# Optimization experiments

Hardware: AMD Instinct MI355X
Metric: run time of the kernel (lower is better)

The kernel has to match this reference:

```python
import jax, jax.numpy as jnp
import numpy as np

B, S, C = 128, 512, 128


def setup_inputs() -> dict:
    key = jax.random.key(0)
    k1, k2, k3, k4, k5 = jax.random.split(key, 5)
    emissions = jax.random.normal(k1, (B, S, C), dtype=jnp.float32)
    tags = jax.random.randint(k2, (B, S), 0, C, dtype=jnp.int64)
    mask = jnp.ones((B, S), dtype=bool)  # mask[:,0] must be True
    transitions = jax.random.normal(k3, (C, C), dtype=jnp.float32)
    start_transitions = jax.random.normal(k4, (C,), dtype=jnp.float32)
    end_transitions = jax.random.normal(k5, (C,), dtype=jnp.float32)
    return {"emissions": emissions, "tags": tags, "mask": mask,
            "transitions": transitions, "start_transitions": start_transitions,
            "end_transitions": end_transitions}


def _gold_score(emissions, tags, mask, transitions, start_t, end_t):
    # score of the gold tag path, fully vectorized over time
    b = jnp.arange(emissions.shape[0])
    score = start_t[tags[:, 0]] + emissions[b, 0, tags[:, 0]]            # [B]
    emit_t = jnp.take_along_axis(emissions, tags[..., None], axis=2)[..., 0]  # [B,S]
    trans_t = transitions[tags[:, :-1], tags[:, 1:]]                     # [B,S-1]
    score = score + jnp.sum((emit_t[:, 1:] + trans_t) * mask[:, 1:].astype(emissions.dtype), axis=1)
    last_idx = jnp.sum(mask.astype(jnp.int32), axis=1) - 1               # [B]
    last_tags = jnp.take_along_axis(tags, last_idx[:, None], axis=1)[:, 0]
    return score + end_t[last_tags]


def _partition(emissions, mask, transitions, start_t, end_t):
    # forward algorithm: sequential logsumexp recurrence via lax.scan
    alpha0 = start_t[None, :] + emissions[:, 0]                          # [B,C]

    def step(alpha, inp):
        emit_t, mask_t = inp                                             # [B,C], [B]
        score = alpha[:, :, None] + transitions[None] + emit_t[:, None, :]  # [B,C,C]
        new_alpha = jax.nn.logsumexp(score, axis=1)                      # [B,C]
        alpha = jnp.where(mask_t[:, None], new_alpha, alpha)
        return alpha, None

    xs = (jnp.moveaxis(emissions[:, 1:], 1, 0), mask[:, 1:].T)           # [S-1,B,C], [S-1,B]
    alpha, _ = jax.lax.scan(step, alpha0, xs)
    return jax.nn.logsumexp(alpha + end_t[None, :], axis=1)              # [B]


def reference(emissions, tags, mask, transitions, start_transitions, end_transitions):
    gold = _gold_score(emissions, tags, mask, transitions, start_transitions, end_transitions)
    part = _partition(emissions, mask, transitions, start_transitions, end_transitions)
    return -(gold - part).mean()
```

## Files before the change

kernel.cpp:

```cpp
#include <hip/hip_runtime.h>

#define BB 128
#define SS 512
#define CC 128

__device__ __forceinline__ void barrier_lgkm() {
    asm volatile("s_waitcnt lgkmcnt(0)" ::: "memory");
    __builtin_amdgcn_s_barrier();
}

__device__ __forceinline__ float lanebcast(float v, int i) {
    return __int_as_float(__builtin_amdgcn_readlane(__float_as_int(v), i));
}

__global__ __launch_bounds__(512, 1)
void crf_half_kernel(const float* __restrict__ emissions,
                     const int*   __restrict__ tags,
                     const float* __restrict__ transitions,
                     const float* __restrict__ start_t,
                     const float* __restrict__ end_t,
                     float* __restrict__ ws)
{
    const int  blk = blockIdx.x;
    const bool isF = (blk < BB);
    const int  b   = isF ? blk : (blk - BB);
    const int  tid = threadIdx.x;
    const int  wv  = tid >> 6;
    const int  q   = wv & 3;
    const int  h   = wv >> 2;
    const int  l   = tid & 63;
    const int  u0  = l & 31;
    const int  j   = h * 64 + l;
    const int  i   = q * 32 + u0;

    float*  gold = ws;
    float*  xf   = ws + BB;
    float*  xb   = xf + BB * CC;
    double* Mf   = (double*)(xb + BB * CC);
    double* Mb   = Mf + BB;

    __shared__ float slot[2][4][CC];
    __shared__ float redg[8];

    const float* em_b = emissions + (size_t)b * SS * CC;

    float Ereg[32];
    {
        const float* Tb = transitions + (isF ? ((size_t)(q * 32) * CC + j)
                                             : ((size_t)j * CC + q * 32));
        const int us = isF ? CC : 1;
        #pragma unroll
        for (int t2 = 0; t2 < 32; ++t2) Ereg[t2] = __expf(Tb[(size_t)t2 * us]);
        #pragma unroll
        for (int t2 = 0; t2 < 32; ++t2) asm volatile("" : "+v"(Ereg[t2]));
    }

    float p = isF ? __expf(start_t[i] + em_b[i])
                  : __expf(end_t[i] + em_b[(size_t)(SS - 1) * CC + i]);
    double M = 0.0;

    const ptrdiff_t em_stride = isF ? (ptrdiff_t)CC : -(ptrdiff_t)CC;
    const float* em_base = em_b + i + (isF ? 3 * CC : 508 * CC);
    float ld0 = em_base[-2 * em_stride];
    float ld1 = em_base[-1 * em_stride];
    float ld2 = em_base[0];

#define SUBSTEP(T_, PAR, IS_BRIDGE) do {                                      \
        float a0=0.f, a1=0.f, a2=0.f, a3=0.f;                                 \
        _Pragma("unroll")                                                     \
        for (int uu = 0; uu < 8; ++uu) {                                      \
            a0 = fmaf(lanebcast(p, 4*uu+0), Ereg[4*uu+0], a0);                \
            a1 = fmaf(lanebcast(p, 4*uu+1), Ereg[4*uu+1], a1);                \
            a2 = fmaf(lanebcast(p, 4*uu+2), Ereg[4*uu+2], a2);                \
            a3 = fmaf(lanebcast(p, 4*uu+3), Ereg[4*uu+3], a3);                \
        }                                                                     \
        slot[PAR][q][j] = (a0 + a1) + (a2 + a3);            \
        float ev = __expf(ld0);                      \
        ld0 = ld1; ld1 = ld2;                                                 \
        ld2 = em_base[(ptrdiff_t)(T_) * em_stride];                           \
        barrier_lgkm();                                                       \
        float s = (slot[PAR][0][i] + slot[PAR][1][i]) +                       \
                  (slot[PAR][2][i] + slot[PAR][3][i]);        \
        float pn = s * ev;                                                    \
        if (!(IS_BRIDGE) && ((T_) & 3) == 1) {                                \
            float r = (slot[PAR][0][0] + slot[PAR][1][0]) +                   \
                      (slot[PAR][2][0] + slot[PAR][3][0]);                    \
            float lr = __logf(r);           \
            M += (double)lr;                                                  \
            pn *= __expf(-lr);                                                \
        }                                                                     \
        if (IS_BRIDGE) pn = s;              \
        p = pn;                                                               \
    } while (0)

    #pragma unroll 1
    for (int t = 1; t < 255; t += 2) {
        SUBSTEP(t,     1, false);
        SUBSTEP(t + 1, 0, false);
    }
    SUBSTEP(255, 1, false);
    if (isF) SUBSTEP(256, 0, true);
#undef SUBSTEP

    if (h == 0 && l < 32) (isF ? xf : xb)[(size_t)b * CC + i] = p;
    if (tid == 0) { if (isF) Mf[b] = M; else Mb[b] = M; }

    if (!isF) {
        const int* tg = tags + b * SS;
        const int t  = tid;
        const int ct = tg[t];
        float g;
        if (t == 0) g = start_t[ct] + em_b[ct] + end_t[tg[SS - 1]];
        else        g = em_b[(size_t)t * CC + ct] + transitions[tg[t - 1] * CC + ct];
        #pragma unroll
        for (int off = 32; off; off >>= 1) g += __shfl_down(g, off);
        if (l == 0) redg[wv] = g;
        __syncthreads();
        if (tid == 0) {
            float gg = 0.f;
            #pragma unroll
            for (int k2 = 0; k2 < 8; ++k2) gg += redg[k2];
            gold[b] = gg;
        }
    }
}

__global__ __launch_bounds__(1024)
void crf_final_kernel(const float* __restrict__ ws, float* __restrict__ out)
{
    const float*  gold = ws;
    const float*  xf   = ws + BB;
    const float*  xb   = xf + BB * CC;
    const double* Mf   = (const double*)(xb + BB * CC);
    const double* Mb   = Mf + BB;

    const int tid = threadIdx.x;
    const int b   = tid >> 3;
    const int g   = tid & 7;

    const float* xa = xf + (size_t)b * CC + g * 16;
    const float* xc = xb + (size_t)b * CC + g * 16;
    float z = 0.f;
    #pragma unroll
    for (int k = 0; k < 16; ++k) z = fmaf(xa[k], xc[k], z);
    z += __shfl_down(z, 4);
    z += __shfl_down(z, 2);
    z += __shfl_down(z, 1);

    __shared__ float d_s[BB];
    __shared__ float red[2];
    if (g == 0) {
        double part = Mf[b] + Mb[b] + (double)__logf(z);
        d_s[b] = gold[b] - (float)part;
    }
    __syncthreads();

    float v = (tid < BB) ? d_s[tid] : 0.f;
    #pragma unroll
    for (int off = 32; off; off >>= 1) v += __shfl_down(v, off);
    if (tid == 0 || tid == 64) red[tid >> 6] = v;
    __syncthreads();
    if (tid == 0) out[0] = -(red[0] + red[1]) / (float)BB;
}

extern "C" void kernel_launch(void* const* d_in, const int* in_sizes, int n_in,
                              void* d_out, int out_size, void* d_ws, size_t ws_size,
                              hipStream_t stream) {
    const float* emissions   = (const float*)d_in[0];
    const int*   tags        = (const int*)d_in[1];
    const float* transitions = (const float*)d_in[3];
    const float* start_t     = (const float*)d_in[4];
    const float* end_t       = (const float*)d_in[5];
    float* out = (float*)d_out;
    float* ws  = (float*)d_ws;

    crf_half_kernel<<<2 * BB, 512, 0, stream>>>(emissions, tags, transitions,
                                                start_t, end_t, ws);
    crf_final_kernel<<<1, 1024, 0, stream>>>(ws, out);
}
```

Measured before the change: 178.8 us.

## Halve workgroup to 256 threads with 64-wide K split per wave

Each block now runs 4 waves instead of 8. Each wave holds 64 exp-transition values and reduces over 64 source states instead of 32, so the cross-wave LDS reduction after the barrier sums 2 partials instead of 4. The emission exp multiply moves before the LDS store, and the gold-score loop processes two timesteps per thread. The aim is a cheaper barrier and reduction per step, at the cost of a longer serial FMA/readlane chain per step and more registers.

Result: faster. 175.1 us (-2.0%).

```diff
diff --git a/kernel.cpp b/kernel.cpp
--- a/kernel.cpp
+++ b/kernel.cpp
@@ -13,7 +13,7 @@
     return __int_as_float(__builtin_amdgcn_readlane(__float_as_int(v), i));
 }
 
-__global__ __launch_bounds__(512, 1)
+__global__ __launch_bounds__(256, 1)
 void crf_half_kernel(const float* __restrict__ emissions,
                      const int*   __restrict__ tags,
                      const float* __restrict__ transitions,
@@ -26,12 +26,11 @@
     const int  b   = isF ? blk : (blk - BB);
     const int  tid = threadIdx.x;
     const int  wv  = tid >> 6;
-    const int  q   = wv & 3;
-    const int  h   = wv >> 2;
+    const int  q   = wv & 1;
+    const int  h   = wv >> 1;
     const int  l   = tid & 63;
-    const int  u0  = l & 31;
     const int  j   = h * 64 + l;
-    const int  i   = q * 32 + u0;
+    const int  i   = q * 64 + l;
 
     float*  gold = ws;
     float*  xf   = ws + BB;
@@ -39,20 +38,20 @@
     double* Mf   = (double*)(xb + BB * CC);
     double* Mb   = Mf + BB;
 
-    __shared__ float slot[2][4][CC];
-    __shared__ float redg[8];
+    __shared__ float slot[2][2][CC];
+    __shared__ float redg[4];
 
     const float* em_b = emissions + (size_t)b * SS * CC;
 
-    float Ereg[32];
+    float Ereg[64];
     {
-        const float* Tb = transitions + (isF ? ((size_t)(q * 32) * CC + j)
-                                             : ((size_t)j * CC + q * 32));
+        const float* Tb = transitions + (isF ? ((size_t)(q * 64) * CC + j)
+                                             : ((size_t)j * CC + q * 64));
         const int us = isF ? CC : 1;
         #pragma unroll
-        for (int t2 = 0; t2 < 32; ++t2) Ereg[t2] = __expf(Tb[(size_t)t2 * us]);
+        for (int t2 = 0; t2 < 64; ++t2) Ereg[t2] = __expf(Tb[(size_t)t2 * us]);
         #pragma unroll
-        for (int t2 = 0; t2 < 32; ++t2) asm volatile("" : "+v"(Ereg[t2]));
+        for (int t2 = 0; t2 < 64; ++t2) asm volatile("" : "+v"(Ereg[t2]));
     }
 
     float p = isF ? __expf(start_t[i] + em_b[i])
@@ -60,7 +59,7 @@
     double M = 0.0;
 
     const ptrdiff_t em_stride = isF ? (ptrdiff_t)CC : -(ptrdiff_t)CC;
-    const float* em_base = em_b + i + (isF ? 3 * CC : 508 * CC);
+    const float* em_base = em_b + j + (isF ? 3 * CC : 508 * CC);
     float ld0 = em_base[-2 * em_stride];
     float ld1 = em_base[-1 * em_stride];
     float ld2 = em_base[0];
@@ -68,28 +67,25 @@
 #define SUBSTEP(T_, PAR, IS_BRIDGE) do {                                      \
         float a0=0.f, a1=0.f, a2=0.f, a3=0.f;                                 \
         _Pragma("unroll")                                                     \
-        for (int uu = 0; uu < 8; ++uu) {                                      \
+        for (int uu = 0; uu < 16; ++uu) {                                     \
             a0 = fmaf(lanebcast(p, 4*uu+0), Ereg[4*uu+0], a0);                \
             a1 = fmaf(lanebcast(p, 4*uu+1), Ereg[4*uu+1], a1);                \
             a2 = fmaf(lanebcast(p, 4*uu+2), Ereg[4*uu+2], a2);                \
             a3 = fmaf(lanebcast(p, 4*uu+3), Ereg[4*uu+3], a3);                \
         }                                                                     \
-        slot[PAR][q][j] = (a0 + a1) + (a2 + a3);            \
-        float ev = __expf(ld0);                      \
+        float part = (a0 + a1) + (a2 + a3);                                   \
+        float ev = (IS_BRIDGE) ? 1.0f : __expf(ld0);                          \
         ld0 = ld1; ld1 = ld2;                                                 \
         ld2 = em_base[(ptrdiff_t)(T_) * em_stride];                           \
+        slot[PAR][q][j] = part * ev;                        \
         barrier_lgkm();                                                       \
-        float s = (slot[PAR][0][i] + slot[PAR][1][i]) +                       \
-                  (slot[PAR][2][i] + slot[PAR][3][i]);        \
-        float pn = s * ev;                                                    \
+        float pn = slot[PAR][0][i] + slot[PAR][1][i];         \
         if (!(IS_BRIDGE) && ((T_) & 3) == 1) {                                \
-            float r = (slot[PAR][0][0] + slot[PAR][1][0]) +                   \
-                      (slot[PAR][2][0] + slot[PAR][3][0]);                    \
-            float lr = __logf(r);           \
+            float r = slot[PAR][0][0] + slot[PAR][1][0];                      \
+            float lr = __logf(r);                   \
             M += (double)lr;                                                  \
             pn *= __expf(-lr);                                                \
         }                                                                     \
-        if (IS_BRIDGE) pn = s;              \
         p = pn;                                                               \
     } while (0)
 
@@ -102,26 +98,25 @@
     if (isF) SUBSTEP(256, 0, true);
 #undef SUBSTEP
 
-    if (h == 0 && l < 32) (isF ? xf : xb)[(size_t)b * CC + i] = p;
+    if (h == 0) (isF ? xf : xb)[(size_t)b * CC + i] = p;
     if (tid == 0) { if (isF) Mf[b] = M; else Mb[b] = M; }
 
     if (!isF) {
         const int* tg = tags + b * SS;
-        const int t  = tid;
-        const int ct = tg[t];
-        float g;
-        if (t == 0) g = start_t[ct] + em_b[ct] + end_t[tg[SS - 1]];
-        else        g = em_b[(size_t)t * CC + ct] + transitions[tg[t - 1] * CC + ct];
+        float g = 0.f;
+        #pragma unroll
+        for (int qq = 0; qq < 2; ++qq) {
+            int t  = tid + qq * 256;
+            int ct = tg[t];
+            if (t == 0) g += start_t[ct] + em_b[ct] + end_t[tg[SS - 1]];
+            else        g += em_b[(size_t)t * CC + ct] +
+                             transitions[tg[t - 1] * CC + ct];
+        }
         #pragma unroll
         for (int off = 32; off; off >>= 1) g += __shfl_down(g, off);
         if (l == 0) redg[wv] = g;
         __syncthreads();
-        if (tid == 0) {
-            float gg = 0.f;
-            #pragma unroll
-            for (int k2 = 0; k2 < 8; ++k2) gg += redg[k2];
-            gold[b] = gg;
-        }
+        if (tid == 0) gold[b] = redg[0] + redg[1] + redg[2] + redg[3];
     }
 }
 
@@ -174,7 +169,7 @@
     float* out = (float*)d_out;
     float* ws  = (float*)d_ws;
 
-    crf_half_kernel<<<2 * BB, 512, 0, stream>>>(emissions, tags, transitions,
+    crf_half_kernel<<<2 * BB, 256, 0, stream>>>(emissions, tags, transitions,
                                                 start_t, end_t, ws);
     crf_final_kernel<<<1, 1024, 0, stream>>>(ws, out);
 }
```
